# Optimization experiments

Hardware: AMD Instinct MI355X
Metric: run time of the kernel (lower is better)

The kernel has to match this reference:

```python
import jax, jax.numpy as jnp
import numpy as np

T_WAV = 1.0 / 16000.0
LOG_F_MEAN = 5.04418
LOG_F_STD = 0.358402


def setup_inputs() -> dict:
    key = jax.random.key(0)
    k1, k2, k3, k4 = jax.random.split(key, 4)
    S, B, M, T, K, D = 16, 16, 20, 640, 16, 80
    x = jax.random.normal(k1, (S, B, M, T), dtype=jnp.float32)
    nlf = jax.random.normal(k2, (S, B, M), dtype=jnp.float32)
    # tau: small time offsets (seconds), within a pitch period
    tau = jax.random.uniform(k3, (S, B, M), dtype=jnp.float32) * 0.01
    W = jax.random.normal(k4, (D, 2 * K), dtype=jnp.float32) * 0.1
    b = jnp.zeros((D,), dtype=jnp.float32)
    return {"x": x, "nlf": nlf, "tau": tau, "W": W, "b": b}


def reference(x, nlf, tau, W, b):
    S, B, M, T = x.shape
    D, twoK = W.shape
    K = twoK // 2
    # nlf -> f (denormalize log-f0 and exponentiate)
    f = jnp.exp(nlf * LOG_F_STD + LOG_F_MEAN)  # [S,B,M]
    # time grid minus tau: [S,B,M,T]
    n_T = jnp.arange(T, dtype=x.dtype) * T_WAV
    t = n_T - tau[..., None]
    # harmonic angular frequencies: k*2pi*f, [S,B,M,K]
    k_2pi = jnp.arange(1, K + 1, dtype=x.dtype) * (2.0 * jnp.pi)
    kf = k_2pi * f[..., None]
    # phase: [S,B,M,K,T]
    deg = kf[..., :, None] * t[..., None, :]
    # contract sin/cos basis against x over T (same math as cat([sin,cos],3) then einsum)
    s_x = jnp.einsum('sbmkt,sbmt->sbmk', jnp.sin(deg), x)
    c_x = jnp.einsum('sbmkt,sbmt->sbmk', jnp.cos(deg), x)
    sin_cos_x = jnp.concatenate([s_x, c_x], axis=-1)  # [S,B,M,2K]
    # fc
    y = jnp.einsum('sbmk,dk->sbmd', sin_cos_x, W) + b  # [S,B,M,D]
    y_SBD = y.reshape(S, B, M * D)
    y_f = jnp.concatenate([y_SBD, nlf], axis=2)  # [S,B,M*D+M]
    h = jax.nn.relu(y_f)
    return h
```

## Files before the change

kernel.cpp:

```cpp
#include <hip/hip_runtime.h>
#include <math.h>


#define T_WAV_F (1.0f / 16000.0f)
#define LOG_F_MEAN_F 5.04418f
#define LOG_F_STD_F 0.358402f

constexpr int S = 16, B = 16, M = 20, T = 640, K = 16, D = 80;
constexpr int ROWS = S * B * M;
constexpr int WPB = 4;
constexpr int TWO_K = 2 * K;
constexpr int W_STRIDE = TWO_K + 1;

__global__ __launch_bounds__(256) void sinenet_kernel(
    const float* __restrict__ x,
    const float* __restrict__ nlf,
    const float* __restrict__ tau,
    const float* __restrict__ W,
    const float* __restrict__ bias,
    float* __restrict__ out)
{
    __shared__ float Wlds[D * W_STRIDE];
    __shared__ float blds[D];

    for (int i = threadIdx.x; i < D * TWO_K; i += 256) {
        Wlds[(i / TWO_K) * W_STRIDE + (i % TWO_K)] = W[i];
    }
    if (threadIdx.x < D) blds[threadIdx.x] = bias[threadIdx.x];
    __syncthreads();

    const int lane = threadIdx.x & 63;
    const int row  = blockIdx.x * WPB + (threadIdx.x >> 6);

    const float* __restrict__ xrow = x + (size_t)row * T;
    const float nlf_v = nlf[row];
    const float tau_v = tau[row];

    const float f    = __expf(fmaf(nlf_v, LOG_F_STD_F, LOG_F_MEAN_F));
    const float drev = f * T_WAV_F;
    const float rev0 = -f * tau_v;

    float sacc[K], cacc[K];
    #pragma unroll
    for (int k = 0; k < K; ++k) { sacc[k] = 0.0f; cacc[k] = 0.0f; }

    #pragma unroll 2
    for (int it = 0; it < T / 64; ++it) {
        const int n = lane + it * 64;
        const float xv = xrow[n];
        const float rev = fmaf((float)n, drev, rev0);
        const float fr  = rev - floorf(rev);
        float s1, c1;
        asm("v_sin_f32 %0, %1" : "=v"(s1) : "v"(fr));
        asm("v_cos_f32 %0, %1" : "=v"(c1) : "v"(fr));
        float zr = c1, zi = s1;
        #pragma unroll
        for (int k = 0; k < K; ++k) {
            sacc[k] = fmaf(xv, zi, sacc[k]);
            cacc[k] = fmaf(xv, zr, cacc[k]);
            const float nzr = fmaf(zr, c1, -(zi * s1));
            const float nzi = fmaf(zr, s1,  (zi * c1));
            zr = nzr; zi = nzi;
        }
    }

    #pragma unroll
    for (int k = 0; k < K; ++k) {
        #pragma unroll
        for (int off = 32; off > 0; off >>= 1) {
            sacc[k] += __shfl_xor(sacc[k], off, 64);
            cacc[k] += __shfl_xor(cacc[k], off, 64);
        }
    }

    const int sb = row / M;
    const int m  = row % M;
    float* __restrict__ orow = out + (size_t)sb * (M * D + M);

    #pragma unroll
    for (int pass = 0; pass < 2; ++pass) {
        const int d = lane + pass * 64;
        if (d < D) {
            const float* __restrict__ wr = &Wlds[d * W_STRIDE];
            float y = blds[d];
            #pragma unroll
            for (int k = 0; k < K; ++k) {
                y = fmaf(sacc[k], wr[k],     y);
                y = fmaf(cacc[k], wr[K + k], y);
            }
            orow[m * D + d] = fmaxf(y, 0.0f);
        }
    }
    if (lane == 0) orow[M * D + m] = fmaxf(nlf_v, 0.0f);
}

extern "C" void kernel_launch(void* const* d_in, const int* in_sizes, int n_in,
                              void* d_out, int out_size, void* d_ws, size_t ws_size,
                              hipStream_t stream) {
    const float* x    = (const float*)d_in[0];
    const float* nlf  = (const float*)d_in[1];
    const float* tau  = (const float*)d_in[2];
    const float* W    = (const float*)d_in[3];
    const float* bias = (const float*)d_in[4];
    float* out = (float*)d_out;

    sinenet_kernel<<<ROWS / WPB, 256, 0, stream>>>(x, nlf, tau, W, bias, out);
}
```

Measured before the change: 82.67 us.

## Use Chebyshev harmonic recurrence and transpose-style butterfly reduction across lanes

Replaces the complex-rotation harmonic recurrence with a Chebyshev three-term recurrence (2cos·s − s_prev), which needs fewer multiplies per harmonic. The 32 separate 6-step wave reductions become a recursive-halving butterfly in which each step exchanges half the remaining values. The first two exchange steps use DPP quad permutes instead of shuffles. Results end up spread across lanes and are gathered with readlane using a bit-reversed index. The loop is fully unrolled and the phase is advanced incrementally, which may slightly change accuracy through accumulated float error and raises register pressure.

```diff
diff --git a/kernel.cpp b/kernel.cpp
--- a/kernel.cpp
+++ b/kernel.cpp
@@ -11,6 +11,19 @@
 constexpr int WPB = 4;
 constexpr int TWO_K = 2 * K;
 constexpr int W_STRIDE = TWO_K + 1;
+
+template <int CTRL>
+__device__ __forceinline__ float dpp_qperm(float x) {
+    return __int_as_float(
+        __builtin_amdgcn_mov_dpp(__float_as_int(x), CTRL, 0xF, 0xF, true));
+}
+
+template <int MASK>
+__device__ __forceinline__ float xsh(float x) {
+    if constexpr (MASK == 1)      return dpp_qperm<0xB1>(x);
+    else if constexpr (MASK == 2) return dpp_qperm<0x4E>(x);
+    else                          return __shfl_xor(x, MASK, 64);
+}
 
 __global__ __launch_bounds__(256) void sinenet_kernel(
     const float* __restrict__ x,
@@ -36,41 +49,81 @@
     const float nlf_v = nlf[row];
     const float tau_v = tau[row];
 
-    const float f    = __expf(fmaf(nlf_v, LOG_F_STD_F, LOG_F_MEAN_F));
-    const float drev = f * T_WAV_F;
-    const float rev0 = -f * tau_v;
+    const float f     = __expf(fmaf(nlf_v, LOG_F_STD_F, LOG_F_MEAN_F));
+    const float drev  = f * T_WAV_F;
+    const float drev64 = 64.0f * drev;
+    float rev = fmaf((float)lane, drev, -f * tau_v);
 
-    float sacc[K], cacc[K];
+    float v[TWO_K];
     #pragma unroll
-    for (int k = 0; k < K; ++k) { sacc[k] = 0.0f; cacc[k] = 0.0f; }
+    for (int j = 0; j < TWO_K; ++j) v[j] = 0.0f;
 
-    #pragma unroll 2
+    #pragma unroll
     for (int it = 0; it < T / 64; ++it) {
-        const int n = lane + it * 64;
-        const float xv = xrow[n];
-        const float rev = fmaf((float)n, drev, rev0);
-        const float fr  = rev - floorf(rev);
-        float s1, c1;
+        const float xv = xrow[lane + it * 64];
+        float fr, s1, c1;
+        asm("v_fract_f32 %0, %1" : "=v"(fr) : "v"(rev));
         asm("v_sin_f32 %0, %1" : "=v"(s1) : "v"(fr));
         asm("v_cos_f32 %0, %1" : "=v"(c1) : "v"(fr));
-        float zr = c1, zi = s1;
+        const float tc = c1 + c1;
+        float sp = 0.0f, s = s1, cp = 1.0f, c = c1;
         #pragma unroll
         for (int k = 0; k < K; ++k) {
-            sacc[k] = fmaf(xv, zi, sacc[k]);
-            cacc[k] = fmaf(xv, zr, cacc[k]);
-            const float nzr = fmaf(zr, c1, -(zi * s1));
-            const float nzi = fmaf(zr, s1,  (zi * c1));
-            zr = nzr; zi = nzi;
+            v[k]     = fmaf(xv, s, v[k]);
+            v[K + k] = fmaf(xv, c, v[K + k]);
+            const float ns = fmaf(tc, s, -sp);
+            const float nc = fmaf(tc, c, -cp);
+            sp = s; s = ns; cp = c; c = nc;
         }
+        rev += drev64;
     }
 
+    {
+        const int l = lane;
+        { const bool hi = l & 1;
+          #pragma unroll
+          for (int j = 0; j < 16; ++j) {
+              const float keep = hi ? v[j + 16] : v[j];
+              const float send = hi ? v[j] : v[j + 16];
+              v[j] = keep + xsh<1>(send);
+          } }
+        { const bool hi = l & 2;
+          #pragma unroll
+          for (int j = 0; j < 8; ++j) {
+              const float keep = hi ? v[j + 8] : v[j];
+              const float send = hi ? v[j] : v[j + 8];
+              v[j] = keep + xsh<2>(send);
+          } }
+        { const bool hi = l & 4;
+          #pragma unroll
+          for (int j = 0; j < 4; ++j) {
+              const float keep = hi ? v[j + 4] : v[j];
+              const float send = hi ? v[j] : v[j + 4];
+              v[j] = keep + xsh<4>(send);
+          } }
+        { const bool hi = l & 8;
+          #pragma unroll
+          for (int j = 0; j < 2; ++j) {
+              const float keep = hi ? v[j + 2] : v[j];
+              const float send = hi ? v[j] : v[j + 2];
+              v[j] = keep + xsh<8>(send);
+          } }
+        { const bool hi = l & 16;
+          const float keep = hi ? v[1] : v[0];
+          const float send = hi ? v[0] : v[1];
+          v[0] = keep + xsh<16>(send);
+        }
+        v[0] += __shfl_xor(v[0], 32, 64);
+    }
+    const float tot = v[0];
+
+    float sv[TWO_K];
     #pragma unroll
-    for (int k = 0; k < K; ++k) {
-        #pragma unroll
-        for (int off = 32; off > 0; off >>= 1) {
-            sacc[k] += __shfl_xor(sacc[k], off, 64);
-            cacc[k] += __shfl_xor(cacc[k], off, 64);
-        }
+    for (int k = 0; k < TWO_K; ++k) {
+        const int src = ((k & 1) << 4) | ((k & 2) << 2) | (k & 4) |
+                        ((k & 8) >> 2) | ((k & 16) >> 4);
+        sv[k] = __int_as_float(
+            __builtin_amdgcn_readlane(__float_as_int(tot), src));
     }
 
     const int sb = row / M;
@@ -84,9 +137,8 @@
             const float* __restrict__ wr = &Wlds[d * W_STRIDE];
             float y = blds[d];
             #pragma unroll
-            for (int k = 0; k < K; ++k) {
-                y = fmaf(sacc[k], wr[k],     y);
-                y = fmaf(cacc[k], wr[K + k], y);
+            for (int j = 0; j < TWO_K; ++j) {
+                y = fmaf(sv[j], wr[j], y);
             }
             orow[m * D + d] = fmaxf(y, 0.0f);
         }
```

Measured after the change: 76.93 us. 6.9% less time.
